# Optimization experiments

Hardware: AMD Instinct MI355X
Metric: run time of the kernel (lower is better)

Reference implementation:

```python
import jax, jax.numpy as jnp
import numpy as np

N = 50000   # nodes
E = 600000  # edges (avg degree 12)
D = 128     # feature dim (input_dim == output_dim for residual)
G = 8       # graphs in batch
EPS = 1e-5


def setup_inputs() -> dict:
    key = jax.random.key(0)
    ks = jax.random.split(key, 8)
    x = jax.random.normal(ks[0], (N, D), dtype=jnp.float32)
    edge_index = jax.random.randint(ks[1], (2, E), 0, N)
    batch = jnp.sort(jax.random.randint(ks[2], (N,), 0, G))
    s = 1.0 / np.sqrt(D)
    Wl = jax.random.normal(ks[3], (D, D), dtype=jnp.float32) * s
    bl = jax.random.normal(ks[4], (D,), dtype=jnp.float32) * s
    Wr = jax.random.normal(ks[5], (D, D), dtype=jnp.float32) * s
    return {
        "x": x,
        "edge_index": edge_index,
        "batch": batch,
        "num_graphs": G,
        "Wl": Wl,
        "bl": bl,
        "Wr": Wr,
        "gn_weight": jnp.ones((D,), jnp.float32),
        "gn_bias": jnp.zeros((D,), jnp.float32),
        "mean_scale": jnp.ones((D,), jnp.float32),
    }


def reference(x, edge_index, batch, num_graphs, Wl, bl, Wr, gn_weight, gn_bias, mean_scale):
    n = x.shape[0]
    src, dst = edge_index[0], edge_index[1]

    # SAGEConv: mean-aggregate neighbor (source) features at target nodes
    ones_e = jnp.ones(src.shape[0], dtype=x.dtype)
    deg = jax.ops.segment_sum(ones_e, dst, num_segments=n)          # [N]
    agg = jax.ops.segment_sum(x[src], dst, num_segments=n)          # [N, D]
    agg = agg / jnp.maximum(deg, 1.0)[:, None]
    f = agg @ Wl.T + bl + x @ Wr.T                                  # lin_l(agg) + lin_r(x)

    # exact (erf) GELU, as torch F.gelu default
    f = jax.nn.gelu(f, approximate=False)

    # GraphNorm: per-graph statistics with learnable mean_scale
    ones_n = jnp.ones(n, dtype=x.dtype)
    cnt = jax.ops.segment_sum(ones_n, batch, num_segments=num_graphs)[:, None]  # [G,1]
    mean = jax.ops.segment_sum(f, batch, num_segments=num_graphs) / cnt         # [G,D]
    out = f - mean_scale * mean[batch]
    var = jax.ops.segment_sum(out * out, batch, num_segments=num_graphs) / cnt  # [G,D]
    out = out / jnp.sqrt(var[batch] + EPS) * gn_weight + gn_bias

    # dropout is identity in eval mode; residual add
    return out + x
```

## Files before the change

kernel.cpp:

```cpp
#include <hip/hip_runtime.h>
#include <hip/hip_bf16.h>

#define D 128
#define NGRAPH 8
#define EPS 1e-5f
#define CAP 48

typedef __attribute__((ext_vector_type(4))) float f32x4;
typedef __attribute__((ext_vector_type(8))) short s16x8;

__device__ __forceinline__ unsigned short f2bf(float f) {
    unsigned int u = __float_as_uint(f);
    u += 0x7fffu + ((u >> 16) & 1u);
    return (unsigned short)(u >> 16);
}
__device__ __forceinline__ float blo(unsigned int u) { return __uint_as_float(u << 16); }
__device__ __forceinline__ float bhi(unsigned int u) { return __uint_as_float(u & 0xffff0000u); }

__global__ __launch_bounds__(256) void prep_fill_kernel(
    const float* __restrict__ Wl, const float* __restrict__ Wr,
    unsigned short* __restrict__ Bsw,
    const float* __restrict__ x, unsigned int* __restrict__ xb,
    const int* __restrict__ batch, int* __restrict__ bnd,
    const int* __restrict__ ei, int* __restrict__ cnt, int* __restrict__ adj,
    int N, int E, int Npad, int fillB)
{
    int b = blockIdx.x;
    if (b < 128) {
        int t = b * 256 + threadIdx.x;
        int j    = t & 7;
        int ln   = (t >> 3) & 63;
        int ks   = (t >> 9) & 7;
        int tile = t >> 12;
        int k = ks * 32 + (ln >> 4) * 8 + j;
        int d = tile * 16 + (ln & 15);
        float v = (k < 128) ? Wl[(size_t)d * 128 + k] : Wr[(size_t)d * 128 + (k - 128)];
        Bsw[t] = f2bf(v);
    } else if (b == 128) {
        int g = threadIdx.x;
        if (g <= NGRAPH) {
            int lo = 0, hi = N;
            while (lo < hi) {
                int mid = (lo + hi) >> 1;
                if (batch[mid] < g) lo = mid + 1; else hi = mid;
            }
            bnd[g] = lo;
        }
    } else if (b < 129 + fillB) {
        int e = (b - 129) * 256 + threadIdx.x;
        if (e < E) {
            int dst = ei[E + e];
            int pos = atomicAdd(&cnt[dst], 1);
            if (pos < CAP) adj[(size_t)dst * CAP + pos] = ei[e];
        }
    } else {
        int iu = (b - 129 - fillB) * 256 + threadIdx.x;
        if (iu < N * 32) {
            float4 p = *(const float4*)(x + (size_t)iu * 4);
            uint2 o;
            o.x = (unsigned int)f2bf(p.x) | ((unsigned int)f2bf(p.y) << 16);
            o.y = (unsigned int)f2bf(p.z) | ((unsigned int)f2bf(p.w) << 16);
            *(uint2*)(xb + (size_t)iu * 2) = o;
        } else if (iu < Npad * 32) {
            *(uint2*)(xb + (size_t)iu * 2) = make_uint2(0u, 0u);
        }
    }
}

__global__ __launch_bounds__(256) void aggregate_kernel(
    const unsigned int* __restrict__ xb, const int* __restrict__ cnt,
    const int* __restrict__ adj, unsigned int* __restrict__ Aag, int N, int Npad)
{
    int n = blockIdx.x * 4 + (threadIdx.x >> 6);
    int lane = threadIdx.x & 63;
    if (n >= Npad) return;
    if (n >= N) { Aag[(size_t)n * 64 + lane] = 0u; return; }
    int deg = cnt[n];
    int lim = deg < CAP ? deg : CAP;
    int v = (lane < lim) ? adj[(size_t)n * CAP + lane] : 0;
    float a0 = 0.0f, a1 = 0.0f;
    int i = 0;
    for (; i + 8 <= lim; i += 8) {
        int nb[8];
#pragma unroll
        for (int k = 0; k < 8; ++k) nb[k] = __shfl(v, i + k, 64);
        unsigned int u[8];
#pragma unroll
        for (int k = 0; k < 8; ++k) u[k] = xb[(size_t)nb[k] * 64 + lane];
#pragma unroll
        for (int k = 0; k < 8; ++k) { a0 += blo(u[k]); a1 += bhi(u[k]); }
    }
    for (; i < lim; ++i) {
        int nb = __shfl(v, i, 64);
        unsigned int u = xb[(size_t)nb * 64 + lane];
        a0 += blo(u); a1 += bhi(u);
    }
    float inv = 1.0f / (float)(deg > 0 ? deg : 1);
    Aag[(size_t)n * 64 + lane] =
        (unsigned int)f2bf(a0 * inv) | ((unsigned int)f2bf(a1 * inv) << 16);
}

__global__ __launch_bounds__(256) void gemm_kernel(
    const unsigned short* __restrict__ Aag, const unsigned short* __restrict__ xb16,
    const unsigned short* __restrict__ Bsw, const float* __restrict__ bl,
    const int* __restrict__ batch,
    float* __restrict__ fout, float* __restrict__ gsum, float* __restrict__ gsumsq,
    int N)
{
    int wave = threadIdx.x >> 6, lane = threadIdx.x & 63;
    int row0 = blockIdx.x * 64 + wave * 16;
    int m = lane & 15, quad = lane >> 4;
    int r = row0 + m;

    s16x8 afrag[8];
    const unsigned short* ab = Aag + (size_t)r * 128 + quad * 8;
#pragma unroll
    for (int ks = 0; ks < 4; ++ks) afrag[ks] = *(const s16x8*)(ab + ks * 32);
    const unsigned short* xp = xb16 + (size_t)r * 128 + quad * 8;
#pragma unroll
    for (int ks = 0; ks < 4; ++ks) afrag[4 + ks] = *(const s16x8*)(xp + ks * 32);

    int nbase = row0;
    bool uni = (nbase + 15 < N) && (batch[nbase] == batch[nbase + 15]);
    int gu = (nbase < N) ? batch[nbase] : 0;

#pragma unroll
    for (int tile = 0; tile < 8; ++tile) {
        f32x4 acc = {0.0f, 0.0f, 0.0f, 0.0f};
        const s16x8* bptr = (const s16x8*)Bsw + (size_t)(tile * 8) * 64 + lane;
#pragma unroll
        for (int ks = 0; ks < 8; ++ks)
            acc = __builtin_amdgcn_mfma_f32_16x16x32_bf16(afrag[ks], bptr[(size_t)ks * 64], acc, 0, 0, 0);
        int d = tile * 16 + m;
        float bias = bl[d];
        float sm = 0.0f, sq = 0.0f;
#pragma unroll
        for (int rr = 0; rr < 4; ++rr) {
            int node = nbase + quad * 4 + rr;
            if (node < N) {
                float v = acc[rr] + bias;
                float g = 0.5f * v * (1.0f + erff(v * 0.70710678118654752f));
                fout[(size_t)node * D + d] = g;
                if (uni) { sm += g; sq += g * g; }
                else {
                    int gg = batch[node];
                    unsafeAtomicAdd(&gsum[gg * D + d], g);
                    unsafeAtomicAdd(&gsumsq[gg * D + d], g * g);
                }
            }
        }
        if (uni) {
            sm += __shfl_xor(sm, 16, 64); sm += __shfl_xor(sm, 32, 64);
            sq += __shfl_xor(sq, 16, 64); sq += __shfl_xor(sq, 32, 64);
            if (quad == 0) {
                unsafeAtomicAdd(&gsum[gu * D + d], sm);
                unsafeAtomicAdd(&gsumsq[gu * D + d], sq);
            }
        }
    }
}

__global__ __launch_bounds__(256) void final_kernel(
    const float* __restrict__ f, const float* __restrict__ x,
    const int* __restrict__ batch, const int* __restrict__ bnd,
    const float* __restrict__ gsum, const float* __restrict__ gsumsq,
    const float* __restrict__ ms,
    const float* __restrict__ gw, const float* __restrict__ gb,
    float* __restrict__ out, int N)
{
    int t = blockIdx.x * 256 + threadIdx.x;
    if (t >= N * (D / 4)) return;
    int n  = t >> 5;
    int d0 = (t & 31) * 4;
    int g  = batch[n];
    int c  = bnd[g + 1] - bnd[g];
    float invc = 1.0f / (float)(c > 0 ? c : 1);
    size_t row = (size_t)n * D + d0;
    float4 fv = *(const float4*)(f + row);
    float4 xv = *(const float4*)(x + row);
    float4 s1 = *(const float4*)(gsum + g * D + d0);
    float4 s2 = *(const float4*)(gsumsq + g * D + d0);
    float4 msv = *(const float4*)(ms + d0);
    float4 gwv = *(const float4*)(gw + d0);
    float4 gbv = *(const float4*)(gb + d0);
    float4 o;
    {
        float mu = s1.x * invc, q = s2.x * invc, a = msv.x * mu;
        float sc = rsqrtf(q - 2.0f * a * mu + a * a + EPS);
        o.x = (fv.x - a) * sc * gwv.x + gbv.x + xv.x;
    }
    {
        float mu = s1.y * invc, q = s2.y * invc, a = msv.y * mu;
        float sc = rsqrtf(q - 2.0f * a * mu + a * a + EPS);
        o.y = (fv.y - a) * sc * gwv.y + gbv.y + xv.y;
    }
    {
        float mu = s1.z * invc, q = s2.z * invc, a = msv.z * mu;
        float sc = rsqrtf(q - 2.0f * a * mu + a * a + EPS);
        o.z = (fv.z - a) * sc * gwv.z + gbv.z + xv.z;
    }
    {
        float mu = s1.w * invc, q = s2.w * invc, a = msv.w * mu;
        float sc = rsqrtf(q - 2.0f * a * mu + a * a + EPS);
        o.w = (fv.w - a) * sc * gwv.w + gbv.w + xv.w;
    }
    *(float4*)(out + row) = o;
}

extern "C" void kernel_launch(void* const* d_in, const int* in_sizes, int n_in,
                              void* d_out, int out_size, void* d_ws, size_t ws_size,
                              hipStream_t stream)
{
    const float* x     = (const float*)d_in[0];
    const int*   ei    = (const int*)d_in[1];
    const int*   batch = (const int*)d_in[2];
    const float* Wl = (const float*)d_in[4];
    const float* bl = (const float*)d_in[5];
    const float* Wr = (const float*)d_in[6];
    const float* gw = (const float*)d_in[7];
    const float* gb = (const float*)d_in[8];
    const float* ms = (const float*)d_in[9];
    float* out = (float*)d_out;

    int N = in_sizes[0] / D;
    int E = in_sizes[1] / 2;
    int NBLK = (N + 63) / 64;
    int Npad = NBLK * 64;

    float*          fout = (float*)d_ws;
    unsigned int*   xb   = (unsigned int*)(fout + (size_t)Npad * D);
    unsigned short* Bsw  = (unsigned short*)(xb + (size_t)Npad * 64);
    float* gsum   = (float*)(Bsw + 32768);
    float* gsumsq = gsum + NGRAPH * D;
    int*   cnt    = (int*)(gsumsq + NGRAPH * D);
    int*   bnd    = cnt + N;
    int*   adj    = bnd + (NGRAPH + 1);
    unsigned int* Aag = (unsigned int*)(adj + (size_t)N * CAP);

    hipMemsetAsync(gsum, 0, (2 * NGRAPH * D) * sizeof(float) + (size_t)N * sizeof(int), stream);

    int fillB = (E + 255) / 256;
    int xbB   = (Npad * 32 + 255) / 256;
    prep_fill_kernel<<<129 + fillB + xbB, 256, 0, stream>>>(
        Wl, Wr, Bsw, x, xb, batch, bnd, ei, cnt, adj, N, E, Npad, fillB);

    aggregate_kernel<<<Npad / 4, 256, 0, stream>>>(xb, cnt, adj, Aag, N, Npad);

    gemm_kernel<<<NBLK, 256, 0, stream>>>(
        (const unsigned short*)Aag, (const unsigned short*)xb, Bsw, bl, batch,
        fout, gsum, gsumsq, N);

    {
        int threads = N * (D / 4);
        final_kernel<<<(threads + 255) / 256, 256, 0, stream>>>(
            fout, x, batch, bnd, gsum, gsumsq, ms, gw, gb, out, N);
    }
}
```

Baseline: 200.4 us.

## Fuse aggregation, GEMM and GraphNorm finalize into one grid-synchronized kernel

Neighbor mean aggregation moves into the GEMM kernel: each lane accumulates its row chunk straight into registers and packs it into bf16 MFMA fragments, so the Aag intermediate is never written or read. When occupancy shows all blocks can be resident at once, a software grid barrier (atomic counter with a spin timeout) lets the same kernel apply GraphNorm and the residual from register-held GELU outputs. This drops the fout round trip and two kernel launches. The cost is a per-row serial gather loop with limited memory parallelism, and a grid barrier that depends on co-residency and falls back on a timeout.

```diff
diff --git a/kernel.cpp b/kernel.cpp
--- a/kernel.cpp
+++ b/kernel.cpp
@@ -1,5 +1,4 @@
 #include <hip/hip_runtime.h>
-#include <hip/hip_bf16.h>
 
 #define D 128
 #define NGRAPH 8
@@ -16,6 +15,13 @@
 }
 __device__ __forceinline__ float blo(unsigned int u) { return __uint_as_float(u << 16); }
 __device__ __forceinline__ float bhi(unsigned int u) { return __uint_as_float(u & 0xffff0000u); }
+
+__device__ __forceinline__ void acc8(float* a, uint4 u) {
+    a[0] += blo(u.x); a[1] += bhi(u.x);
+    a[2] += blo(u.y); a[3] += bhi(u.y);
+    a[4] += blo(u.z); a[5] += bhi(u.z);
+    a[6] += blo(u.w); a[7] += bhi(u.w);
+}
 
 __global__ __launch_bounds__(256) void prep_fill_kernel(
     const float* __restrict__ Wl, const float* __restrict__ Wr,
@@ -67,56 +73,57 @@
     }
 }
 
-__global__ __launch_bounds__(256) void aggregate_kernel(
+template<int COOP>
+__global__ __launch_bounds__(256, 4) void fused_kernel(
     const unsigned int* __restrict__ xb, const int* __restrict__ cnt,
-    const int* __restrict__ adj, unsigned int* __restrict__ Aag, int N, int Npad)
-{
-    int n = blockIdx.x * 4 + (threadIdx.x >> 6);
-    int lane = threadIdx.x & 63;
-    if (n >= Npad) return;
-    if (n >= N) { Aag[(size_t)n * 64 + lane] = 0u; return; }
-    int deg = cnt[n];
-    int lim = deg < CAP ? deg : CAP;
-    int v = (lane < lim) ? adj[(size_t)n * CAP + lane] : 0;
-    float a0 = 0.0f, a1 = 0.0f;
-    int i = 0;
-    for (; i + 8 <= lim; i += 8) {
-        int nb[8];
-#pragma unroll
-        for (int k = 0; k < 8; ++k) nb[k] = __shfl(v, i + k, 64);
-        unsigned int u[8];
-#pragma unroll
-        for (int k = 0; k < 8; ++k) u[k] = xb[(size_t)nb[k] * 64 + lane];
-#pragma unroll
-        for (int k = 0; k < 8; ++k) { a0 += blo(u[k]); a1 += bhi(u[k]); }
-    }
-    for (; i < lim; ++i) {
-        int nb = __shfl(v, i, 64);
-        unsigned int u = xb[(size_t)nb * 64 + lane];
-        a0 += blo(u); a1 += bhi(u);
-    }
-    float inv = 1.0f / (float)(deg > 0 ? deg : 1);
-    Aag[(size_t)n * 64 + lane] =
-        (unsigned int)f2bf(a0 * inv) | ((unsigned int)f2bf(a1 * inv) << 16);
-}
-
-__global__ __launch_bounds__(256) void gemm_kernel(
-    const unsigned short* __restrict__ Aag, const unsigned short* __restrict__ xb16,
-    const unsigned short* __restrict__ Bsw, const float* __restrict__ bl,
-    const int* __restrict__ batch,
-    float* __restrict__ fout, float* __restrict__ gsum, float* __restrict__ gsumsq,
-    int N)
+    const int* __restrict__ adj, const unsigned short* __restrict__ Bsw,
+    const float* __restrict__ bl, const int* __restrict__ batch,
+    const int* __restrict__ bnd, const float* __restrict__ x,
+    const float* __restrict__ ms, const float* __restrict__ gw,
+    const float* __restrict__ gb,
+    float* __restrict__ gsum, float* __restrict__ gsumsq,
+    unsigned int* __restrict__ bar, float* __restrict__ fout,
+    float* __restrict__ out, int N)
 {
     int wave = threadIdx.x >> 6, lane = threadIdx.x & 63;
     int row0 = blockIdx.x * 64 + wave * 16;
     int m = lane & 15, quad = lane >> 4;
     int r = row0 + m;
 
+    float ag[4][8];
+#pragma unroll
+    for (int ks = 0; ks < 4; ++ks)
+#pragma unroll
+        for (int j = 0; j < 8; ++j) ag[ks][j] = 0.0f;
+
+    int deg = (r < N) ? cnt[r] : 0;
+    int lim = deg < CAP ? deg : CAP;
+    const int* arow = adj + (size_t)r * CAP;
+    int nb = (lim > 0) ? arow[0] : 0;
+    for (int i = 0; i < lim; ++i) {
+        int nbn = (i + 1 < lim) ? arow[i + 1] : 0;
+        const uint4* rowp = (const uint4*)(xb + (size_t)nb * 64);
+        uint4 u0 = rowp[quad];
+        uint4 u1 = rowp[quad + 4];
+        uint4 u2 = rowp[quad + 8];
+        uint4 u3 = rowp[quad + 12];
+        acc8(ag[0], u0);
+        acc8(ag[1], u1);
+        acc8(ag[2], u2);
+        acc8(ag[3], u3);
+        nb = nbn;
+    }
+    float inv = 1.0f / (float)(deg > 0 ? deg : 1);
+
     s16x8 afrag[8];
-    const unsigned short* ab = Aag + (size_t)r * 128 + quad * 8;
-#pragma unroll
-    for (int ks = 0; ks < 4; ++ks) afrag[ks] = *(const s16x8*)(ab + ks * 32);
-    const unsigned short* xp = xb16 + (size_t)r * 128 + quad * 8;
+#pragma unroll
+    for (int ks = 0; ks < 4; ++ks) {
+        s16x8 a;
+#pragma unroll
+        for (int j = 0; j < 8; ++j) a[j] = (short)f2bf(ag[ks][j] * inv);
+        afrag[ks] = a;
+    }
+    const unsigned short* xp = (const unsigned short*)xb + (size_t)r * 128 + quad * 8;
 #pragma unroll
     for (int ks = 0; ks < 4; ++ks) afrag[4 + ks] = *(const s16x8*)(xp + ks * 32);
 
@@ -124,6 +131,7 @@
     bool uni = (nbase + 15 < N) && (batch[nbase] == batch[nbase + 15]);
     int gu = (nbase < N) ? batch[nbase] : 0;
 
+    float val[8][4];
 #pragma unroll
     for (int tile = 0; tile < 8; ++tile) {
         f32x4 acc = {0.0f, 0.0f, 0.0f, 0.0f};
@@ -137,10 +145,10 @@
 #pragma unroll
         for (int rr = 0; rr < 4; ++rr) {
             int node = nbase + quad * 4 + rr;
+            float v = acc[rr] + bias;
+            float g = 0.5f * v * (1.0f + erff(v * 0.70710678118654752f));
+            val[tile][rr] = g;
             if (node < N) {
-                float v = acc[rr] + bias;
-                float g = 0.5f * v * (1.0f + erff(v * 0.70710678118654752f));
-                fout[(size_t)node * D + d] = g;
                 if (uni) { sm += g; sq += g * g; }
                 else {
                     int gg = batch[node];
@@ -155,6 +163,76 @@
             if (quad == 0) {
                 unsafeAtomicAdd(&gsum[gu * D + d], sm);
                 unsafeAtomicAdd(&gsumsq[gu * D + d], sq);
+            }
+        }
+    }
+
+    if constexpr (!COOP) {
+#pragma unroll
+        for (int tile = 0; tile < 8; ++tile) {
+            int d = tile * 16 + m;
+#pragma unroll
+            for (int rr = 0; rr < 4; ++rr) {
+                int node = nbase + quad * 4 + rr;
+                if (node < N) fout[(size_t)node * D + d] = val[tile][rr];
+            }
+        }
+        return;
+    }
+
+    __syncthreads();
+    if (threadIdx.x == 0) {
+        __hip_atomic_fetch_add(bar, 1u, __ATOMIC_ACQ_REL, __HIP_MEMORY_SCOPE_AGENT);
+        unsigned long long t0 = __builtin_amdgcn_s_memrealtime();
+        while (__hip_atomic_load(bar, __ATOMIC_RELAXED, __HIP_MEMORY_SCOPE_AGENT) < gridDim.x) {
+            __builtin_amdgcn_s_sleep(10);
+            if (__builtin_amdgcn_s_memrealtime() - t0 > 5000000ull) break;
+        }
+    }
+    __syncthreads();
+
+    int node0 = nbase + quad * 4;
+    if (node0 < N) {
+        int last = (node0 + 3 < N - 1) ? node0 + 3 : N - 1;
+        int g0 = batch[node0];
+        int gL = batch[last];
+        if (g0 == gL) {
+            int c = bnd[g0 + 1] - bnd[g0];
+            float invc = 1.0f / (float)(c > 0 ? c : 1);
+#pragma unroll
+            for (int tile = 0; tile < 8; ++tile) {
+                int d = tile * 16 + m;
+                float s1 = __hip_atomic_load(&gsum[g0 * D + d], __ATOMIC_RELAXED, __HIP_MEMORY_SCOPE_AGENT);
+                float s2 = __hip_atomic_load(&gsumsq[g0 * D + d], __ATOMIC_RELAXED, __HIP_MEMORY_SCOPE_AGENT);
+                float mu = s1 * invc, q = s2 * invc, a = ms[d] * mu;
+                float sc = rsqrtf(q - 2.0f * a * mu + a * a + EPS);
+                float gwv = gw[d], gbv = gb[d];
+#pragma unroll
+                for (int rr = 0; rr < 4; ++rr) {
+                    int node = node0 + rr;
+                    if (node < N)
+                        out[(size_t)node * D + d] =
+                            (val[tile][rr] - a) * sc * gwv + gbv + x[(size_t)node * D + d];
+                }
+            }
+        } else {
+#pragma unroll
+            for (int rr = 0; rr < 4; ++rr) {
+                int node = node0 + rr;
+                if (node >= N) continue;
+                int g = batch[node];
+                int c = bnd[g + 1] - bnd[g];
+                float invc = 1.0f / (float)(c > 0 ? c : 1);
+#pragma unroll
+                for (int tile = 0; tile < 8; ++tile) {
+                    int d = tile * 16 + m;
+                    float s1 = __hip_atomic_load(&gsum[g * D + d], __ATOMIC_RELAXED, __HIP_MEMORY_SCOPE_AGENT);
+                    float s2 = __hip_atomic_load(&gsumsq[g * D + d], __ATOMIC_RELAXED, __HIP_MEMORY_SCOPE_AGENT);
+                    float mu = s1 * invc, q = s2 * invc, a = ms[d] * mu;
+                    float sc = rsqrtf(q - 2.0f * a * mu + a * a + EPS);
+                    out[(size_t)node * D + d] =
+                        (val[tile][rr] - a) * sc * gw[d] + gb[d] + x[(size_t)node * D + d];
+                }
             }
         }
     }
@@ -232,25 +310,37 @@
     unsigned short* Bsw  = (unsigned short*)(xb + (size_t)Npad * 64);
     float* gsum   = (float*)(Bsw + 32768);
     float* gsumsq = gsum + NGRAPH * D;
-    int*   cnt    = (int*)(gsumsq + NGRAPH * D);
+    unsigned int* bar = (unsigned int*)(gsumsq + NGRAPH * D);
+    int*   cnt    = (int*)(bar + 4);
     int*   bnd    = cnt + N;
     int*   adj    = bnd + (NGRAPH + 1);
-    unsigned int* Aag = (unsigned int*)(adj + (size_t)N * CAP);
-
-    hipMemsetAsync(gsum, 0, (2 * NGRAPH * D) * sizeof(float) + (size_t)N * sizeof(int), stream);
+
+    hipMemsetAsync(gsum, 0,
+                   (2 * NGRAPH * D) * sizeof(float) + 4 * sizeof(unsigned int)
+                   + (size_t)N * sizeof(int), stream);
 
     int fillB = (E + 255) / 256;
     int xbB   = (Npad * 32 + 255) / 256;
     prep_fill_kernel<<<129 + fillB + xbB, 256, 0, stream>>>(
         Wl, Wr, Bsw, x, xb, batch, bnd, ei, cnt, adj, N, E, Npad, fillB);
 
-    aggregate_kernel<<<Npad / 4, 256, 0, stream>>>(xb, cnt, adj, Aag, N, Npad);
-
-    gemm_kernel<<<NBLK, 256, 0, stream>>>(
-        (const unsigned short*)Aag, (const unsigned short*)xb, Bsw, bl, batch,
-        fout, gsum, gsumsq, N);
-
-    {
+    int occ = 0, ncu = 0, dev = 0;
+    bool coop = false;
+    if (hipOccupancyMaxActiveBlocksPerMultiprocessor(&occ, fused_kernel<1>, 256, 0) == hipSuccess) {
+        if (hipGetDevice(&dev) != hipSuccess) dev = 0;
+        if (hipDeviceGetAttribute(&ncu, hipDeviceAttributeMultiprocessorCount, dev) != hipSuccess || ncu <= 0)
+            ncu = 256;
+        coop = ((long long)occ * (long long)ncu >= (long long)NBLK);
+    }
+
+    if (coop) {
+        fused_kernel<1><<<NBLK, 256, 0, stream>>>(
+            xb, cnt, adj, Bsw, bl, batch, bnd, x, ms, gw, gb,
+            gsum, gsumsq, bar, fout, out, N);
+    } else {
+        fused_kernel<0><<<NBLK, 256, 0, stream>>>(
+            xb, cnt, adj, Bsw, bl, batch, bnd, x, ms, gw, gb,
+            gsum, gsumsq, bar, fout, out, N);
         int threads = N * (D / 4);
         final_kernel<<<(threads + 255) / 256, 256, 0, stream>>>(
             fout, x, batch, bnd, gsum, gsumsq, ms, gw, gb, out, N);
```

Measured after the change: 192.7 us. 1.04x faster.

## Gather neighbor features in FP8 and split GEMM output tiles across waves

Applied to the files above, without the earlier changes.

The prep kernel now also writes an FP8 (e4m3) copy of x into the fout buffer region, and the aggregation gathers 2 bytes per lane instead of 4, then decodes with the hardware FP8-to-FP32 conversion. This halves the bytes moved by the random neighbor gather, at the cost of mean-aggregation accuracy, since x is quantized to FP8 before averaging. The GEMM kernel now covers 32 rows per block, with two waves per 16-row group each computing 4 of the 8 output tiles, and declares an occupancy hint of 8. The goal is more parallelism and less per-wave work. The erf GELU is also computed before the bounds check.

```diff
diff --git a/kernel.cpp b/kernel.cpp
--- a/kernel.cpp
+++ b/kernel.cpp
@@ -1,5 +1,4 @@
 #include <hip/hip_runtime.h>
-#include <hip/hip_bf16.h>
 
 #define D 128
 #define NGRAPH 8
@@ -7,6 +6,7 @@
 #define CAP 48
 
 typedef __attribute__((ext_vector_type(4))) float f32x4;
+typedef __attribute__((ext_vector_type(2))) float f32x2;
 typedef __attribute__((ext_vector_type(8))) short s16x8;
 
 __device__ __forceinline__ unsigned short f2bf(float f) {
@@ -14,13 +14,12 @@
     u += 0x7fffu + ((u >> 16) & 1u);
     return (unsigned short)(u >> 16);
 }
-__device__ __forceinline__ float blo(unsigned int u) { return __uint_as_float(u << 16); }
-__device__ __forceinline__ float bhi(unsigned int u) { return __uint_as_float(u & 0xffff0000u); }
 
 __global__ __launch_bounds__(256) void prep_fill_kernel(
     const float* __restrict__ Wl, const float* __restrict__ Wr,
     unsigned short* __restrict__ Bsw,
     const float* __restrict__ x, unsigned int* __restrict__ xb,
+    unsigned int* __restrict__ xf8,
     const int* __restrict__ batch, int* __restrict__ bnd,
     const int* __restrict__ ei, int* __restrict__ cnt, int* __restrict__ adj,
     int N, int E, int Npad, int fillB)
@@ -55,20 +54,27 @@
         }
     } else {
         int iu = (b - 129 - fillB) * 256 + threadIdx.x;
-        if (iu < N * 32) {
-            float4 p = *(const float4*)(x + (size_t)iu * 4);
-            uint2 o;
-            o.x = (unsigned int)f2bf(p.x) | ((unsigned int)f2bf(p.y) << 16);
-            o.y = (unsigned int)f2bf(p.z) | ((unsigned int)f2bf(p.w) << 16);
-            *(uint2*)(xb + (size_t)iu * 2) = o;
-        } else if (iu < Npad * 32) {
-            *(uint2*)(xb + (size_t)iu * 2) = make_uint2(0u, 0u);
+        if (iu < Npad * 32) {
+            int n = iu >> 5, slot = iu & 31;
+            if (iu < N * 32) {
+                float4 p = *(const float4*)(x + (size_t)iu * 4);
+                uint2 o;
+                o.x = (unsigned int)f2bf(p.x) | ((unsigned int)f2bf(p.y) << 16);
+                o.y = (unsigned int)f2bf(p.z) | ((unsigned int)f2bf(p.w) << 16);
+                *(uint2*)(xb + (size_t)iu * 2) = o;
+                int u8 = __builtin_amdgcn_cvt_pk_fp8_f32(p.x, p.y, 0, false);
+                u8     = __builtin_amdgcn_cvt_pk_fp8_f32(p.z, p.w, u8, true);
+                xf8[(size_t)n * 32 + slot] = (unsigned int)u8;
+            } else {
+                *(uint2*)(xb + (size_t)iu * 2) = make_uint2(0u, 0u);
+                xf8[(size_t)n * 32 + slot] = 0u;
+            }
         }
     }
 }
 
 __global__ __launch_bounds__(256) void aggregate_kernel(
-    const unsigned int* __restrict__ xb, const int* __restrict__ cnt,
+    const unsigned short* __restrict__ xf8, const int* __restrict__ cnt,
     const int* __restrict__ adj, unsigned int* __restrict__ Aag, int N, int Npad)
 {
     int n = blockIdx.x * 4 + (threadIdx.x >> 6);
@@ -84,31 +90,36 @@
         int nb[8];
 #pragma unroll
         for (int k = 0; k < 8; ++k) nb[k] = __shfl(v, i + k, 64);
-        unsigned int u[8];
-#pragma unroll
-        for (int k = 0; k < 8; ++k) u[k] = xb[(size_t)nb[k] * 64 + lane];
-#pragma unroll
-        for (int k = 0; k < 8; ++k) { a0 += blo(u[k]); a1 += bhi(u[k]); }
+        unsigned short u[8];
+#pragma unroll
+        for (int k = 0; k < 8; ++k) u[k] = xf8[(size_t)nb[k] * 64 + lane];
+#pragma unroll
+        for (int k = 0; k < 8; ++k) {
+            f32x2 d2 = __builtin_amdgcn_cvt_pk_f32_fp8((int)(unsigned int)u[k], false);
+            a0 += d2[0]; a1 += d2[1];
+        }
     }
     for (; i < lim; ++i) {
         int nb = __shfl(v, i, 64);
-        unsigned int u = xb[(size_t)nb * 64 + lane];
-        a0 += blo(u); a1 += bhi(u);
+        f32x2 d2 = __builtin_amdgcn_cvt_pk_f32_fp8(
+            (int)(unsigned int)xf8[(size_t)nb * 64 + lane], false);
+        a0 += d2[0]; a1 += d2[1];
     }
     float inv = 1.0f / (float)(deg > 0 ? deg : 1);
     Aag[(size_t)n * 64 + lane] =
         (unsigned int)f2bf(a0 * inv) | ((unsigned int)f2bf(a1 * inv) << 16);
 }
 
-__global__ __launch_bounds__(256) void gemm_kernel(
+__global__ __launch_bounds__(256, 8) void gemm_kernel(
     const unsigned short* __restrict__ Aag, const unsigned short* __restrict__ xb16,
     const unsigned short* __restrict__ Bsw, const float* __restrict__ bl,
     const int* __restrict__ batch,
-    float* __restrict__ fout, float* __restrict__ gsum, float* __restrict__ gsumsq,
-    int N)
+    float* __restrict__ gsum, float* __restrict__ gsumsq,
+    float* __restrict__ fout, int N)
 {
     int wave = threadIdx.x >> 6, lane = threadIdx.x & 63;
-    int row0 = blockIdx.x * 64 + wave * 16;
+    int row0 = blockIdx.x * 32 + (wave >> 1) * 16;
+    int th = wave & 1;
     int m = lane & 15, quad = lane >> 4;
     int r = row0 + m;
 
@@ -125,7 +136,8 @@
     int gu = (nbase < N) ? batch[nbase] : 0;
 
 #pragma unroll
-    for (int tile = 0; tile < 8; ++tile) {
+    for (int t = 0; t < 4; ++t) {
+        int tile = th * 4 + t;
         f32x4 acc = {0.0f, 0.0f, 0.0f, 0.0f};
         const s16x8* bptr = (const s16x8*)Bsw + (size_t)(tile * 8) * 64 + lane;
 #pragma unroll
@@ -137,9 +149,9 @@
 #pragma unroll
         for (int rr = 0; rr < 4; ++rr) {
             int node = nbase + quad * 4 + rr;
+            float v = acc[rr] + bias;
+            float g = 0.5f * v * (1.0f + erff(v * 0.70710678118654752f));
             if (node < N) {
-                float v = acc[rr] + bias;
-                float g = 0.5f * v * (1.0f + erff(v * 0.70710678118654752f));
                 fout[(size_t)node * D + d] = g;
                 if (uni) { sm += g; sq += g * g; }
                 else {
@@ -226,29 +238,35 @@
     int E = in_sizes[1] / 2;
     int NBLK = (N + 63) / 64;
     int Npad = NBLK * 64;
+    int NB32 = Npad / 32;
 
     float*          fout = (float*)d_ws;
+    unsigned int*   xf8  = (unsigned int*)fout;
     unsigned int*   xb   = (unsigned int*)(fout + (size_t)Npad * D);
     unsigned short* Bsw  = (unsigned short*)(xb + (size_t)Npad * 64);
     float* gsum   = (float*)(Bsw + 32768);
     float* gsumsq = gsum + NGRAPH * D;
-    int*   cnt    = (int*)(gsumsq + NGRAPH * D);
+    unsigned int* pad = (unsigned int*)(gsumsq + NGRAPH * D);
+    int*   cnt    = (int*)(pad + 4);
     int*   bnd    = cnt + N;
     int*   adj    = bnd + (NGRAPH + 1);
     unsigned int* Aag = (unsigned int*)(adj + (size_t)N * CAP);
 
-    hipMemsetAsync(gsum, 0, (2 * NGRAPH * D) * sizeof(float) + (size_t)N * sizeof(int), stream);
+    hipMemsetAsync(gsum, 0,
+                   (2 * NGRAPH * D) * sizeof(float) + 4 * sizeof(unsigned int)
+                   + (size_t)N * sizeof(int), stream);
 
     int fillB = (E + 255) / 256;
     int xbB   = (Npad * 32 + 255) / 256;
     prep_fill_kernel<<<129 + fillB + xbB, 256, 0, stream>>>(
-        Wl, Wr, Bsw, x, xb, batch, bnd, ei, cnt, adj, N, E, Npad, fillB);
-
-    aggregate_kernel<<<Npad / 4, 256, 0, stream>>>(xb, cnt, adj, Aag, N, Npad);
-
-    gemm_kernel<<<NBLK, 256, 0, stream>>>(
-        (const unsigned short*)Aag, (const unsigned short*)xb, Bsw, bl, batch,
-        fout, gsum, gsumsq, N);
+        Wl, Wr, Bsw, x, xb, xf8, batch, bnd, ei, cnt, adj, N, E, Npad, fillB);
+
+    aggregate_kernel<<<Npad / 4, 256, 0, stream>>>(
+        (const unsigned short*)xf8, cnt, adj, Aag, N, Npad);
+
+    gemm_kernel<<<NB32, 256, 0, stream>>>(
+        (const unsigned short*)Aag, (const unsigned short*)xb, Bsw, bl,
+        batch, gsum, gsumsq, fout, N);
 
     {
         int threads = N * (D / 4);
```

Measured after the change: 193.5 us. 3.4% less time.
